# Kernel optimization log

Measured on AMD Instinct MI355X. Metric: run time of the kernel, lower is better.

The kernel has to match this reference:

```python
import jax, jax.numpy as jnp
import numpy as np

SR = 22050
L = 2097153            # output_size = int(SR*95.109); equals NFFT//2+1 so spectral broadcast is well-defined
NFFT = 4194304         # 2**ceil(log2(L))
BANDS = [(1.0, 4.0), (4.0, 8.0), (8.0, 13.0), (13.0, 30.0), (30.0, 100.0), (100.0, 200.0)]
SPEC = [7.83, 528.0, 396.0, 2.5, 14.1, 432.0, 6.0, 30.0]
WIN = 15               # min(15, NFFT//100)
FREQS_NP = np.fft.rfftfreq(NFFT, 1.0 / SR).astype(np.float32)
FREQS = jnp.asarray(FREQS_NP)


def _freq_mod(sig, band_w, freq_w, harm_prog, tm_w1, tm_b1, tm_w2, tm_b2, tm_w3, tm_b3):
    t = jnp.arange(L, dtype=jnp.float32)
    Xf = jnp.fft.rfft(jnp.pad(sig, (0, NFFT - L)))            # [L] complex64
    # sequential band enhancements == product of per-band multipliers
    mult = jnp.ones((L,), jnp.float32)
    for b, (lo, hi) in enumerate(BANDS):
        c = (lo + hi) / 2.0
        w = (hi - lo) / 2.0
        mask = jnp.exp(-0.5 * ((FREQS - c) / (w / 2.0)) ** 2)
        mask = jnp.where((FREQS < lo) | (FREQS > hi), 0.0, mask)
        tmod = jnp.sin(2.0 * np.pi * c * t / SR)
        mult = mult * (1.0 + mask * band_w[b] * (1.0 + 0.2 * tmod))
    # harmonic progression (identical for every specific frequency -> compute once)
    tn = (t / L)[:, None]
    h = jax.nn.relu(tn @ tm_w1 + tm_b1)
    h = jax.nn.relu(h @ tm_w2 + tm_b2)
    mp = h @ tm_w3 + tm_b3                                    # [L, 8]
    chord_idx = jnp.floor(t / L * 8.0).astype(jnp.int32) % 8
    chord = harm_prog[chord_idx] * (1.0 + mp[:, 1] * jnp.sin(2.0 * np.pi * t / L))[:, None]
    prog_mean = chord.mean()
    # specific-frequency harmonic windows (static indices; commutative multiplies)
    smult = jnp.ones((L,), jnp.float32)
    for k, f in enumerate(SPEC):
        for m in (1.0, 2.0, 3.0, 4.0, 5.0):
            hf = f * m
            if hf >= SR / 2:
                continue
            hidx = int(np.argmin(np.abs(FREQS_NP - hf)))
            s = max(0, hidx - WIN)
            e = min(L - 1, hidx + WIN)
            win = jnp.asarray(np.exp(-0.5 * ((np.arange(s, e + 1) - hidx) / (WIN / 3.0)) ** 2).astype(np.float32))
            enh = freq_w[k] * win * (1.0 / m ** 1.2) * (1.0 + prog_mean)
            smult = smult.at[s:e + 1].multiply(1.0 + enh)
    Xf = Xf * mult * smult
    mag = jnp.abs(Xf)
    ph = jnp.angle(Xf)
    mag_s = jnp.concatenate([mag[:1], mag[1:-1] * 0.7 + mag[:-2] * 0.15 + mag[2:] * 0.15, mag[-1:]])
    Xc = mag_s * jnp.exp(1j * ph)
    return jnp.fft.irfft(Xc, n=NFFT)[:L]


def _conv1d(x, w, b, stride):
    y = jax.lax.conv_general_dilated(x, w, (stride,), [(2, 2)], dimension_numbers=("NCH", "OIH", "NCH"))
    return y + b[None, :, None]


def setup_inputs() -> dict:
    key = jax.random.key(0)
    ks = jax.random.split(key, 16)
    n = lambda k, s, sc=1.0: jax.random.normal(k, s, dtype=jnp.float32) * sc
    return {
        "z": n(ks[0], (1, 1, L)),
        "condition": n(ks[1], (1, 8)),
        "band_w": jnp.full((6,), 0.5, jnp.float32),
        "freq_w": jnp.full((8,), 0.3, jnp.float32),
        "harm_prog": n(ks[2], (8, 4)),
        "tm_w1": n(ks[3], (1, 32), 0.5), "tm_b1": jnp.zeros((32,), jnp.float32),
        "tm_w2": n(ks[4], (32, 16), 0.2), "tm_b2": jnp.zeros((16,), jnp.float32),
        "tm_w3": n(ks[5], (16, 8), 0.2), "tm_b3": jnp.zeros((8,), jnp.float32),
        "c1_w": n(ks[6], (32, 1, 5), 0.3), "c1_b": jnp.zeros((32,), jnp.float32),
        "c2_w": n(ks[7], (64, 32, 5), 0.08), "c2_b": jnp.zeros((64,), jnp.float32),
        "c3_w": n(ks[8], (128, 64, 5), 0.05), "c3_b": jnp.zeros((128,), jnp.float32),
        "mx_w1": n(ks[9], (192, 256), 0.07), "mx_b1": jnp.zeros((256,), jnp.float32),
        "mx_w2": n(ks[10], (256, 1), 0.06), "mx_b2": jnp.zeros((1,), jnp.float32),
    }


def reference(z, condition, band_w, freq_w, harm_prog, tm_w1, tm_b1, tm_w2, tm_b2, tm_w3, tm_b3,
              c1_w, c1_b, c2_w, c2_b, c3_w, c3_b, mx_w1, mx_b1, mx_w2, mx_b2):
    base = _freq_mod(z[0, 0], band_w, freq_w, harm_prog, tm_w1, tm_b1, tm_w2, tm_b2, tm_w3, tm_b3)[None, None, :]
    h = jax.nn.leaky_relu(_conv1d(base, c1_w, c1_b, 2), 0.2)
    h = jax.nn.leaky_relu(_conv1d(h, c2_w, c2_b, 2), 0.2)
    h = jax.nn.leaky_relu(_conv1d(h, c3_w, c3_b, 2), 0.2)
    feat = h.mean(axis=2)                                     # [1, 128]
    emb = jnp.zeros((1, 64), jnp.float32)                     # instrument_idx=None path
    mixed = jnp.concatenate([feat, emb], axis=1)              # [1, 192]
    out = jax.nn.leaky_relu(mixed @ mx_w1 + mx_b1, 0.2) @ mx_w2 + mx_b2
    return out
```

## Files before the change

kernel.cpp:

```cpp
#include <hip/hip_runtime.h>
#include <cmath>

#define LSIG  2097153
#define MH    2097152
#define NFFTC 4194304
#define NT128 16384
#define O1C   1048577
#define O2C   524289
#define O3C   262145

#define TO3   62
#define NB3   4229

#define A_OFF    0
#define B_OFF    16777216
#define PM_OFF   58720268
#define FEAT_OFF 58720272
#define W2Q_OFF  50331664
#define W3Q_OFF  50352144
#define W1Q_OFF  50434064

struct SmultTab { int hidx[40]; float inv12[40]; int fk[40]; int maxe; };

typedef short short8 __attribute__((ext_vector_type(8)));
typedef float f32x4v __attribute__((ext_vector_type(4)));

union AFrag { uint4 q; short8 s; };
union BFrag { uint4 q; unsigned int u[4]; short8 s; };

__device__ __forceinline__ float lrelu(float a){ return a > 0.0f ? a : 0.2f*a; }

__device__ __forceinline__ float hsin(float rev){ return __builtin_amdgcn_sinf(rev); }
__device__ __forceinline__ float hcos(float rev){ return __builtin_amdgcn_cosf(rev); }

__device__ __forceinline__ unsigned int rbf(float f) {
  unsigned int u = __float_as_uint(f);
  u += 0x7fffu + ((u >> 16) & 1u);
  return u >> 16;
}
__device__ __forceinline__ unsigned int pack_bf2(float a, float b) {
  unsigned int r;
  asm("v_cvt_pk_bf16_f32 %0, %1, %2" : "=v"(r) : "v"(a), "v"(b));
  return r;
}

__device__ __forceinline__ int swz1(int pos, int dw) {
  return (pos*16 + dw) ^ (((pos >> 1) & 7) << 2);
}
__device__ __forceinline__ int swz2(int pos, int dw) {
  return (pos*32 + dw) ^ (((pos >> 1) & 7) << 2);
}

__device__ __forceinline__ float2 cadd(float2 a, float2 b){ return make_float2(a.x+b.x, a.y+b.y); }
__device__ __forceinline__ float2 csub(float2 a, float2 b){ return make_float2(a.x-b.x, a.y-b.y); }

template<bool FWD> __device__ __forceinline__ float2 jrot(float2 z){
  return FWD ? make_float2(z.y, -z.x) : make_float2(-z.y, z.x);
}

template<bool FWD> __device__ __forceinline__ void dft8(float2 v[8]) {
  const float cq = 0.70710678118654752440f;
  const float S  = FWD ? -1.0f : 1.0f;
  float2 e0 = cadd(v[0], v[4]), e1 = csub(v[0], v[4]);
  float2 e2 = cadd(v[2], v[6]), e3 = csub(v[2], v[6]);
  float2 E0 = cadd(e0, e2), E2 = csub(e0, e2);
  float2 jt = jrot<FWD>(e3);
  float2 E1 = cadd(e1, jt), E3 = csub(e1, jt);
  float2 o0 = cadd(v[1], v[5]), o1 = csub(v[1], v[5]);
  float2 o2 = cadd(v[3], v[7]), o3 = csub(v[3], v[7]);
  float2 O0 = cadd(o0, o2), O2 = csub(o0, o2);
  float2 jo = jrot<FWD>(o3);
  float2 O1 = cadd(o1, jo), O3 = csub(o1, jo);
  float2 w1 = make_float2(cq*O1.x - S*cq*O1.y, cq*O1.y + S*cq*O1.x);
  float2 w2 = jrot<FWD>(O2);
  float2 w3 = make_float2(-cq*O3.x - S*cq*O3.y, -cq*O3.y + S*cq*O3.x);
  v[0] = cadd(E0, O0); v[4] = csub(E0, O0);
  v[1] = cadd(E1, w1); v[5] = csub(E1, w1);
  v[2] = cadd(E2, w2); v[6] = csub(E2, w2);
  v[3] = cadd(E3, w3); v[7] = csub(E3, w3);
}

template<bool FWD>
__device__ __forceinline__ void fft128_body(float2* stage, int t, int jb, int Ns) {
  const float ssg = FWD ? -1.0f : 1.0f;
  const float invden = 1.0f / (float)(128 * Ns);
  {
    const int jj = t >> 4, b = t & 15;
    const int m = (jb + jj) & (Ns - 1);
    float2 v[8];
#pragma unroll
    for (int a = 0; a < 8; ++a) {
      const int r = 16*a + b;
      float2 x = stage[jj*128 + ((r + 9*jj) & 127)];
      if (Ns > 1) {
        float rev = (float)(m * r) * invden;
        float sn = ssg * hsin(rev), cs = hcos(rev);
        x = make_float2(x.x*cs - x.y*sn, x.x*sn + x.y*cs);
      }
      v[a] = x;
    }
    dft8<FWD>(v);
#pragma unroll
    for (int d = 0; d < 8; ++d)
      stage[jj*128 + ((16*d + b + 9*jj) & 127)] = v[d];
  }
  __syncthreads();
  {
    float2 y[16];
    const int jj = (t & 255) >> 3, d = t & 7;
    if (t < 256) {
#pragma unroll
      for (int b = 0; b < 16; ++b) {
        float2 x = stage[jj*128 + ((16*d + b + 9*jj) & 127)];
        float rev = (float)(b*d) * 0.0078125f;
        float sn = ssg * hsin(rev), cs = hcos(rev);
        y[b] = make_float2(x.x*cs - x.y*sn, x.x*sn + x.y*cs);
      }
    }
    __syncthreads();
    if (t < 256) {
      float2 E[8], O[8];
#pragma unroll
      for (int b = 0; b < 8; ++b) { E[b] = y[2*b]; O[b] = y[2*b+1]; }
      dft8<FWD>(E);
      dft8<FWD>(O);
#pragma unroll
      for (int c = 0; c < 8; ++c) {
        float rev = (float)c * 0.0625f;
        float sn = ssg * hsin(rev), cs = hcos(rev);
        float2 To = make_float2(O[c].x*cs - O[c].y*sn, O[c].x*sn + O[c].y*cs);
        stage[jj*128 + ((8*c + d + 9*jj) & 127)]      = cadd(E[c], To);
        stage[jj*128 + ((8*c + 64 + d + 9*jj) & 127)] = csub(E[c], To);
      }
    }
  }
  __syncthreads();
}

template<bool FWD, bool TRUNC>
__global__ __launch_bounds__(512) void kfft128(const float2* __restrict__ src,
                                               float2* __restrict__ dst, int Ns) {
  __shared__ float2 stage[4096];
  const int t = threadIdx.x;
  const int jb = blockIdx.x * 32;
  for (int c = 0; c < 8; ++c) {
    int idx = t + 512*c;
    int jj = idx & 31, rr = idx >> 5;
    stage[jj*128 + ((rr + 9*jj) & 127)] = src[jb + jj + rr*NT128];
  }
  __syncthreads();
  fft128_body<FWD>(stage, t, jb, Ns);
  for (int c = 0; c < 8; ++c) {
    int idx = t + 512*c;
    int jj, k;
    if (Ns == 1) { jj = idx >> 7; k = idx & 127; }
    else         { jj = idx & 31; k = idx >> 5; }
    int j2 = jb + jj, m2 = j2 & (Ns - 1);
    if (TRUNC && !(k < 64 || (k == 64 && j2 == 0))) continue;
    dst[(j2 - m2)*128 + m2 + k*Ns] = stage[jj*128 + ((k + 9*jj) & 127)];
  }
}

__global__ __launch_bounds__(512) void kfirst(
    const float* __restrict__ zin, float2* __restrict__ dst,
    const float* __restrict__ tw1, const float* __restrict__ tb1,
    const float* __restrict__ tw2, const float* __restrict__ tb2,
    const float* __restrict__ tw3, const float* __restrict__ tb3,
    const float* __restrict__ hp, float* __restrict__ pm,
    float* __restrict__ feat) {
  __shared__ float2 stage[4096];
  __shared__ float sw1[32], sb1[32], sw2[512], sb2[16], sw3[16], shp[8], sb31[1];
  __shared__ float red[512];
  const int t = threadIdx.x;
  const int bb = blockIdx.x;
  if (bb < 512) {
    const int jb = bb * 32;
    for (int c = 0; c < 8; ++c) {
      int idx = t + 512*c;
      int jj = idx & 31, rr = idx >> 5;
      int n = jb + jj + rr*NT128;
      float2 a;
      if (n < 1048576)       a = ((const float2*)zin)[n];
      else if (n == 1048576) a = make_float2(zin[2097152], 0.0f);
      else                   a = make_float2(0.0f, 0.0f);
      stage[jj*128 + ((rr + 9*jj) & 127)] = a;
    }
    __syncthreads();
    fft128_body<true>(stage, t, jb, 1);
    for (int c = 0; c < 8; ++c) {
      int idx = t + 512*c;
      int jj = idx >> 7, k = idx & 127;
      dst[(jb + jj)*128 + k] = stage[jj*128 + ((k + 9*jj) & 127)];
    }
    return;
  }
  if (t < 32) { sw1[t] = tw1[t]; sb1[t] = tb1[t]; }
  sw2[t] = tw2[t];
  if (t < 16) { sb2[t] = tb2[t]; sw3[t] = tw3[t*8+1]; }
  if (t < 8) { float s = 0.f; for (int j = 0; j < 4; ++j) s += hp[t*4+j]; shp[t] = s; }
  if (t == 0) sb31[0] = tb3[1];
  __syncthreads();
  const int gid = (bb - 512)*512 + t;
  if (gid < 32768) feat[gid] = 0.0f;
  const float Lf = 2097153.0f;
  float tnv[4], sv[4];
  int ci[4];
  float acc[4][16];
#pragma unroll
  for (int e = 0; e < 4; ++e) {
    float ti = (float)(gid + e*524288);
    float tn = ti / Lf;
    tnv[e] = tn;
    sv[e] = hsin(tn);
    ci[e] = ((int)floorf(tn * 8.0f)) & 7;
#pragma unroll
    for (int kk = 0; kk < 16; ++kk) acc[e][kk] = sb2[kk];
  }
  for (int j = 0; j < 32; ++j) {
    float a = sw1[j], b = sb1[j];
    float hj[4];
#pragma unroll
    for (int e = 0; e < 4; ++e) hj[e] = fmaxf(a*tnv[e] + b, 0.0f);
#pragma unroll
    for (int kk = 0; kk < 16; ++kk) {
      float w = sw2[j*16 + kk];
#pragma unroll
      for (int e = 0; e < 4; ++e) acc[e][kk] += hj[e]*w;
    }
  }
  float lsum = 0.0f;
#pragma unroll
  for (int e = 0; e < 4; ++e) {
    float mp1 = sb31[0];
#pragma unroll
    for (int kk = 0; kk < 16; ++kk) mp1 += fmaxf(acc[e][kk], 0.0f)*sw3[kk];
    lsum += shp[ci[e]] * (1.0f + mp1*sv[e]);
  }
  if (gid == 0) {
    float ti = 2097152.0f;
    float tn = ti / Lf;
    float a1[16];
    for (int kk = 0; kk < 16; ++kk) a1[kk] = sb2[kk];
    for (int j = 0; j < 32; ++j) {
      float h = fmaxf(sw1[j]*tn + sb1[j], 0.0f);
      for (int kk = 0; kk < 16; ++kk) a1[kk] += h*sw2[j*16+kk];
    }
    float mp1 = sb31[0];
    for (int kk = 0; kk < 16; ++kk) mp1 += fmaxf(a1[kk], 0.0f)*sw3[kk];
    float svx = hsin(tn);
    int cix = ((int)floorf(tn * 8.0f)) & 7;
    lsum += shp[cix] * (1.0f + mp1*svx);
  }
  red[t] = lsum;
  __syncthreads();
  for (int off = 256; off > 0; off >>= 1) {
    if (t < off) red[t] += red[t+off];
    __syncthreads();
  }
  if (t == 0) atomicAdd(pm, red[0]);
}

__device__ __forceinline__ float2 xsplit(float2 zk, float2 zm, float rev) {
  float2 s  = make_float2(zk.x + zm.x, zk.y - zm.y);
  float2 dd = make_float2(zk.x - zm.x, zk.y + zm.y);
  float sn = -hsin(rev), cs = hcos(rev);
  float2 t1 = make_float2(cs*dd.x - sn*dd.y, cs*dd.y + sn*dd.x);
  return make_float2(0.5f*(s.x + t1.y), 0.5f*(s.y - t1.x));
}
__device__ __forceinline__ float2 scale_xc(float2 c, float mg, float ms) {
  if (mg > 0.0f) { float sc = ms/mg; return make_float2(c.x*sc, c.y*sc); }
  return make_float2(ms, 0.0f);
}
__device__ __forceinline__ float2 invpack(int n, float2 a, float2 b) {
  float2 s  = make_float2(a.x + b.x, a.y - b.y);
  float2 dd = make_float2(a.x - b.x, a.y + b.y);
  float rev = (float)n * (1.0f / (float)NFFTC);
  float sn = hsin(rev), cs = hcos(rev);
  float2 xo = make_float2(0.5f*(cs*dd.x - sn*dd.y), 0.5f*(cs*dd.y + sn*dd.x));
  const float sc = 1.0f / (float)MH;
  return make_float2((0.5f*s.x - xo.y)*sc, (0.5f*s.y + xo.x)*sc);
}

__global__ __launch_bounds__(256) void kspectral(const float2* __restrict__ Z,
    float2* __restrict__ A, const float* __restrict__ bwp,
    const float* __restrict__ fwp, const float* __restrict__ pm_in, SmultTab tab,
    const float* __restrict__ c1w, const float* __restrict__ c2w,
    const float* __restrict__ c3w, unsigned short* __restrict__ w1q,
    unsigned short* __restrict__ w2q, unsigned short* __restrict__ w3q) {
  const int bb = blockIdx.x;
  const int t = threadIdx.x;
  if (bb >= 4096) {
    int i = (bb - 4096)*256 + t;
    if (i < 1024) {
      int e = i & 7, quad = (i >> 3) & 3, ch = i >> 5;
      float v = (quad == 0 && e < 5) ? c1w[ch*5 + e] : 0.0f;
      w1q[i] = (unsigned short)rbf(v);
    }
    if (i < 10240) {
      int e = i & 7, quad = (i >> 3) & 3, kt = (i >> 5) % 5, ch = i / 160;
      int c1 = quad*8 + e;
      w2q[i] = (unsigned short)rbf(c2w[ch*160 + c1*5 + kt]);
    }
    if (i < 40960) {
      int e = i & 7, quad = (i >> 3) & 3, kt = (i >> 5) % 10, ch = i / 320;
      int c2 = (kt & 1)*32 + quad*8 + e;
      w3q[i] = (unsigned short)rbf(c3w[ch*320 + c2*5 + (kt >> 1)]);
    }
    return;
  }
  __shared__ float2 Xlo[258], Xhi[258];
  __shared__ float  Mlo[258], Mhi[258];
  const int k0 = bb * 256;
  const float pm1 = 1.0f + pm_in[0] * (1.0f/8388612.0f);
  for (int w = t; w < 258; w += 256) {
    int k = k0 - 1 + w;
    float2 zk = Z[k & (MH-1)];
    float2 zm = Z[(MH - k) & (MH-1)];
    {
      float2 X = xsplit(zk, zm, (float)k * (1.0f/(float)NFFTC));
      float mv = 1.0f;
      if (k <= 38050) {
        const float blo[6] = {1.0f,4.0f,8.0f,13.0f,30.0f,100.0f};
        const float bhi[6] = {4.0f,8.0f,13.0f,30.0f,100.0f,200.0f};
        const float bcn[6] = {2.5f,6.0f,10.5f,21.5f,65.0f,150.0f};
        const float bhw[6] = {0.75f,1.0f,1.25f,4.25f,17.5f,25.0f};
        float f = (float)((double)k * (22050.0/4194304.0));
#pragma unroll
        for (int b = 0; b < 6; ++b) {
          if (f >= blo[b] && f <= bhi[b]) {
            float q = (f - bcn[b]) / bhw[b];
            float mask = expf(-0.5f*q*q);
            double frd = (double)k * ((double)bcn[b] / 22050.0);
            frd -= floor(frd);
            float tm = hsin((float)frd);
            mv *= (1.0f + mask * bwp[b] * (1.0f + 0.2f*tm));
          }
        }
      }
      if (k <= tab.maxe) {
        for (int ww = 0; ww < 40; ++ww) {
          int dlt = k - tab.hidx[ww];
          if (dlt >= -15 && dlt <= 15) {
            float x = (float)dlt * 0.2f;
            float win = expf(-0.5f*x*x);
            float enh = fwp[tab.fk[ww]] * win * tab.inv12[ww] * pm1;
            mv *= (1.0f + enh);
          }
        }
      }
      X.x *= mv; X.y *= mv;
      Xlo[w] = X; Mlo[w] = sqrtf(X.x*X.x + X.y*X.y);
    }
    {
      float2 X = xsplit(zm, zk, (float)(MH - k) * (1.0f/(float)NFFTC));
      Xhi[w] = X; Mhi[w] = sqrtf(X.x*X.x + X.y*X.y);
    }
  }
  __syncthreads();
  const int k = k0 + t, w = t + 1;
  float msl = (k == 0) ? Mlo[w] : 0.7f*Mlo[w] + 0.15f*(Mlo[w-1] + Mlo[w+1]);
  float2 xl = scale_xc(Xlo[w], Mlo[w], msl);
  float msh = (k == 0) ? Mhi[w] : 0.7f*Mhi[w] + 0.15f*(Mhi[w+1] + Mhi[w-1]);
  float2 xh = scale_xc(Xhi[w], Mhi[w], msh);
  A[k] = invpack(k, xl, xh);
  if (k >= 1) A[MH - k] = invpack(MH - k, xh, xl);
  if (bb == 4095 && t == 255) {
    float2 Xm = Xlo[257]; float Mm = Mlo[257];
    float ms = 0.7f*Mm + 0.15f*(Mlo[256] + Mhi[256]);
    float2 xm = scale_xc(Xm, Mm, ms);
    A[1048576] = invpack(1048576, xm, xm);
  }
}

__global__ __launch_bounds__(256, 4) void kconv(const float* __restrict__ x,
    const unsigned short* __restrict__ w1q, const unsigned short* __restrict__ w2q,
    const unsigned short* __restrict__ w3q, const float* __restrict__ c1b,
    const float* __restrict__ c2b, const float* __restrict__ c3b,
    float* __restrict__ feat) {
  __shared__ float sb[552];
  __shared__ unsigned int sh1[4352];
  __shared__ unsigned int sh2[4224];
  const int tid  = threadIdx.x;
  const int blk  = blockIdx.x;
  const int s3   = blk * TO3;
  const int lane = tid & 63;
  const int wv   = tid >> 6;
  const int col  = lane & 15;
  const int quad = lane >> 4;

  const uint4* W1 = (const uint4*)w1q;
  AFrag a1w[2];
#pragma unroll
  for (int mi = 0; mi < 2; ++mi)
    a1w[mi].q = W1[(mi*16 + col)*4 + quad];

  const uint4* W2 = (const uint4*)w2q;
  const int mt2 = (wv & 1) * 2;
  const int ntb2 = (wv >> 1) * 4;
  uint4 wk2[2][5];
#pragma unroll
  for (int mi = 0; mi < 2; ++mi)
#pragma unroll
    for (int kt = 0; kt < 5; ++kt)
      wk2[mi][kt] = W2[(((mt2+mi)*16 + col)*5 + kt)*4 + quad];

  float b1r[2][4], b2r[2][4];
#pragma unroll
  for (int mi = 0; mi < 2; ++mi)
#pragma unroll
    for (int r = 0; r < 4; ++r) {
      b1r[mi][r] = c1b[mi*16 + quad*4 + r];
      b2r[mi][r] = c2b[(mt2+mi)*16 + quad*4 + r];
    }

  {
    const int pb = 8*s3 - 14;
    for (int idx = tid; idx < 552; idx += 256) {
      int p = pb + idx;
      sb[idx] = (idx < 517 && p >= 0 && p < LSIG) ? x[p] : 0.0f;
    }
    if (tid < 128) sh2[4096 + tid] = 0u;
  }
  __syncthreads();

  {
    const int a1 = 4*s3 - 6;
    for (int nt = wv; nt < 17; nt += 4) {
      const int n = nt*16 + col;
      BFrag bf;
      if (quad == 0) {
        const float* ps = &sb[2*n];
        bf.u[0] = pack_bf2(ps[0], ps[1]);
        bf.u[1] = pack_bf2(ps[2], ps[3]);
        bf.u[2] = pack_bf2(ps[4], ps[5]);
        bf.u[3] = pack_bf2(ps[6], ps[7]);
      } else {
        bf.u[0] = 0u; bf.u[1] = 0u; bf.u[2] = 0u; bf.u[3] = 0u;
      }
      f32x4v acc[2];
      acc[0] = (f32x4v){b1r[0][0], b1r[0][1], b1r[0][2], b1r[0][3]};
      acc[1] = (f32x4v){b1r[1][0], b1r[1][1], b1r[1][2], b1r[1][3]};
      acc[0] = __builtin_amdgcn_mfma_f32_16x16x32_bf16(a1w[0].s, bf.s, acc[0], 0, 0, 0);
      acc[1] = __builtin_amdgcn_mfma_f32_16x16x32_bf16(a1w[1].s, bf.s, acc[1], 0, 0, 0);
      const int o1 = a1 + n;
      const bool ok = (n <= 257) && (o1 >= 0) && (o1 < O1C);
#pragma unroll
      for (int mi = 0; mi < 2; ++mi) {
        float v0 = ok ? lrelu(acc[mi][0]) : 0.0f;
        float v1 = ok ? lrelu(acc[mi][1]) : 0.0f;
        float v2 = ok ? lrelu(acc[mi][2]) : 0.0f;
        float v3 = ok ? lrelu(acc[mi][3]) : 0.0f;
        uint2 pk; pk.x = pack_bf2(v0, v1); pk.y = pack_bf2(v2, v3);
        *(uint2*)&sh1[swz1(n, mi*8 + quad*2)] = pk;
      }
    }
  }
  __syncthreads();

  f32x4v acc2[2][4];
#pragma unroll
  for (int mi = 0; mi < 2; ++mi)
#pragma unroll
    for (int nt = 0; nt < 4; ++nt)
      acc2[mi][nt] = (f32x4v){b2r[mi][0], b2r[mi][1], b2r[mi][2], b2r[mi][3]};
#pragma unroll
  for (int kt = 0; kt < 5; ++kt) {
#pragma unroll
    for (int nt = 0; nt < 4; ++nt) {
      const int n = (ntb2 + nt)*16 + col;
      const int row = 2*n + kt;
      BFrag bf;
      bf.q = *(const uint4*)&sh1[swz1(row, quad*4)];
      AFrag a0, a1; a0.q = wk2[0][kt]; a1.q = wk2[1][kt];
      acc2[0][nt] = __builtin_amdgcn_mfma_f32_16x16x32_bf16(a0.s, bf.s, acc2[0][nt], 0, 0, 0);
      acc2[1][nt] = __builtin_amdgcn_mfma_f32_16x16x32_bf16(a1.s, bf.s, acc2[1][nt], 0, 0, 0);
    }
  }

  {
    const int a2 = 2*s3 - 2;
#pragma unroll
    for (int nt = 0; nt < 4; ++nt) {
      const int p = (ntb2 + nt)*16 + col;
      const int o2 = a2 + p;
      const bool ok = (o2 >= 0) && (o2 < O2C);
#pragma unroll
      for (int mi = 0; mi < 2; ++mi) {
        float v0 = ok ? lrelu(acc2[mi][nt][0]) : 0.0f;
        float v1 = ok ? lrelu(acc2[mi][nt][1]) : 0.0f;
        float v2 = ok ? lrelu(acc2[mi][nt][2]) : 0.0f;
        float v3 = ok ? lrelu(acc2[mi][nt][3]) : 0.0f;
        const int dwb = (mt2+mi)*8 + quad*2;
        uint2 pk; pk.x = pack_bf2(v0, v1); pk.y = pack_bf2(v2, v3);
        *(uint2*)&sh2[swz2(p, dwb)] = pk;
      }
    }
  }
  __syncthreads();

  {
    const uint4* W3 = (const uint4*)w3q;
    const int slot = (blk & 255) * 128;
#pragma unroll
    for (int pass = 0; pass < 2; ++pass) {
      const int mt = wv + 4*pass;
      uint4 wk3[10];
#pragma unroll
      for (int kt = 0; kt < 10; ++kt)
        wk3[kt] = W3[((mt*16 + col)*10 + kt)*4 + quad];
      float b3r[4];
#pragma unroll
      for (int r = 0; r < 4; ++r) b3r[r] = c3b[mt*16 + quad*4 + r];
      f32x4v acc3[4];
#pragma unroll
      for (int nt = 0; nt < 4; ++nt)
        acc3[nt] = (f32x4v){b3r[0], b3r[1], b3r[2], b3r[3]};
#pragma unroll
      for (int kt = 0; kt < 10; ++kt) {
        const int tap = kt >> 1;
        const int hh  = (kt & 1) * 16;
#pragma unroll
        for (int nt = 0; nt < 4; ++nt) {
          const int n = nt*16 + col;
          const int row = 2*n + tap;
          BFrag bf;
          bf.q = *(const uint4*)&sh2[swz2(row, hh + quad*4)];
          AFrag a; a.q = wk3[kt];
          acc3[nt] = __builtin_amdgcn_mfma_f32_16x16x32_bf16(a.s, bf.s, acc3[nt], 0, 0, 0);
        }
      }
#pragma unroll
      for (int r = 0; r < 4; ++r) {
        const int ch = mt*16 + quad*4 + r;
        float v = 0.0f;
#pragma unroll
        for (int nt = 0; nt < 4; ++nt) {
          const int n = nt*16 + col;
          const bool ok = (n < TO3) && (s3 + n < O3C);
          if (ok) v += lrelu(acc3[nt][r]);
        }
        v += __shfl_xor(v, 1);
        v += __shfl_xor(v, 2);
        v += __shfl_xor(v, 4);
        v += __shfl_xor(v, 8);
        if (col == 0) atomicAdd(&feat[slot + ch], v);
      }
    }
  }
}

__global__ __launch_bounds__(256) void kfinal(const float* __restrict__ feat,
    const float* __restrict__ mw1, const float* __restrict__ mb1,
    const float* __restrict__ mw2, const float* __restrict__ mb2,
    float* __restrict__ out) {
  __shared__ float sfeat[128];
  __shared__ float red[256];
  const int tid = threadIdx.x;
  if (tid < 128) {
    float s = 0.0f;
    for (int sl = 0; sl < 256; ++sl) s += feat[sl*128 + tid];
    sfeat[tid] = s / 262145.0f;
  }
  __syncthreads();
  float y = mb1[tid];
  for (int i = 0; i < 128; ++i) y += sfeat[i] * mw1[i*256 + tid];
  y = y > 0.0f ? y : 0.2f*y;
  red[tid] = y * mw2[tid];
  __syncthreads();
  for (int off = 128; off > 0; off >>= 1) {
    if (tid < off) red[tid] += red[tid+off];
    __syncthreads();
  }
  if (tid == 0) out[0] = red[0] + mb2[0];
}

extern "C" void kernel_launch(void* const* d_in, const int* in_sizes, int n_in,
                              void* d_out, int out_size, void* d_ws, size_t ws_size,
                              hipStream_t stream) {
  (void)in_sizes; (void)n_in; (void)out_size; (void)ws_size;
  const float* z   = (const float*)d_in[0];
  const float* bw  = (const float*)d_in[2];
  const float* fw  = (const float*)d_in[3];
  const float* hp  = (const float*)d_in[4];
  const float* tw1 = (const float*)d_in[5];
  const float* tb1 = (const float*)d_in[6];
  const float* tw2 = (const float*)d_in[7];
  const float* tb2 = (const float*)d_in[8];
  const float* tw3 = (const float*)d_in[9];
  const float* tb3 = (const float*)d_in[10];
  const float* c1w = (const float*)d_in[11];
  const float* c1b = (const float*)d_in[12];
  const float* c2w = (const float*)d_in[13];
  const float* c2b = (const float*)d_in[14];
  const float* c3w = (const float*)d_in[15];
  const float* c3b = (const float*)d_in[16];
  const float* mw1 = (const float*)d_in[17];
  const float* mb1 = (const float*)d_in[18];
  const float* mw2 = (const float*)d_in[19];
  const float* mb2 = (const float*)d_in[20];

  char* wsb = (char*)d_ws;
  float2* A    = (float2*)(wsb + A_OFF);
  float2* B    = (float2*)(wsb + B_OFF);
  float*  PM   = (float*)(wsb + PM_OFF);
  float*  FEAT = (float*)(wsb + FEAT_OFF);
  unsigned short* W1Q = (unsigned short*)(wsb + W1Q_OFF);
  unsigned short* W2Q = (unsigned short*)(wsb + W2Q_OFF);
  unsigned short* W3Q = (unsigned short*)(wsb + W3Q_OFF);

  SmultTab tab;
  {
    const double spec[8] = {7.83, 528.0, 396.0, 2.5, 14.1, 432.0, 6.0, 30.0};
    int n = 0, maxe = 0;
    for (int kk = 0; kk < 8; ++kk)
      for (int m = 1; m <= 5; ++m) {
        double hf = spec[kk] * (double)m;
        if (hf >= 11025.0) continue;
        int hidx = (int)std::floor(hf * (4194304.0/22050.0) + 0.5);
        tab.hidx[n]  = hidx;
        tab.inv12[n] = (float)(1.0/std::pow((double)m, 1.2));
        tab.fk[n]    = kk;
        if (hidx + 15 > maxe) maxe = hidx + 15;
        ++n;
      }
    tab.maxe = maxe;
  }

  (void)hipMemsetAsync(wsb + PM_OFF, 0, 4, stream);

  kfirst<<<1536,512,0,stream>>>(z, A, tw1,tb1,tw2,tb2,tw3,tb3,hp, PM, FEAT);

  kfft128<true,false><<<512,512,0,stream>>>(A, B, 128);
  kfft128<true,false><<<512,512,0,stream>>>(B, A, 16384);

  kspectral<<<4256,256,0,stream>>>(A, B, bw, fw, PM, tab, c1w, c2w, c3w, W1Q, W2Q, W3Q);

  kfft128<false,false><<<512,512,0,stream>>>(B, A, 1);
  kfft128<false,false><<<512,512,0,stream>>>(A, B, 128);
  kfft128<false,true ><<<512,512,0,stream>>>(B, A, 16384);

  kconv<<<NB3,256,0,stream>>>((const float*)A, W1Q, W2Q, W3Q, c1b, c2b, c3b, FEAT);
  kfinal<<<1,256,0,stream>>>(FEAT, mw1, mb1, mw2, mb2, (float*)d_out);
}
```

Baseline: 278.8 us.

## Fuse two inverse FFT passes into one 16K-point shared-memory kernel with transposed spectral output

The spectral kernel now handles 2048 bins per block and writes its inverse-packed output in transposed column order. A new 1024-thread kernel can then run a full 16384-point inverse FFT per column entirely in a 128 KB shared-memory tile, replacing two separate global-memory passes. Shared-memory slot indexing in the existing FFT kernels also gains an XOR swizzle to reduce bank conflicts. This removes one full read and write of the 4M-point complex array. In exchange, only 128 blocks run with one block per CU, which can leave the GPU underoccupied, and the transposed scattered writes may coalesce poorly.

```diff
diff --git a/kernel.cpp b/kernel.cpp
--- a/kernel.cpp
+++ b/kernel.cpp
@@ -49,6 +49,15 @@
 }
 __device__ __forceinline__ int swz2(int pos, int dw) {
   return (pos*32 + dw) ^ (((pos >> 1) & 7) << 2);
+}
+
+__device__ __forceinline__ int slot128(int jj, int q) {
+  int s = q ^ ((q >> 4) & 7);
+  return jj*128 + ((s + 9*jj) & 127);
+}
+__device__ __forceinline__ int phys16k(int x) {
+  int hi = x >> 7, lo = x & 127;
+  return hi*128 + (((lo + 9*hi) & 127) ^ ((hi >> 4) & 7));
 }
 
 __device__ __forceinline__ float2 cadd(float2 a, float2 b){ return make_float2(a.x+b.x, a.y+b.y); }
@@ -91,7 +100,7 @@
 #pragma unroll
     for (int a = 0; a < 8; ++a) {
       const int r = 16*a + b;
-      float2 x = stage[jj*128 + ((r + 9*jj) & 127)];
+      float2 x = stage[slot128(jj, r)];
       if (Ns > 1) {
         float rev = (float)(m * r) * invden;
         float sn = ssg * hsin(rev), cs = hcos(rev);
@@ -102,7 +111,7 @@
     dft8<FWD>(v);
 #pragma unroll
     for (int d = 0; d < 8; ++d)
-      stage[jj*128 + ((16*d + b + 9*jj) & 127)] = v[d];
+      stage[slot128(jj, 16*d + b)] = v[d];
   }
   __syncthreads();
   {
@@ -111,7 +120,7 @@
     if (t < 256) {
 #pragma unroll
       for (int b = 0; b < 16; ++b) {
-        float2 x = stage[jj*128 + ((16*d + b + 9*jj) & 127)];
+        float2 x = stage[slot128(jj, 16*d + b)];
         float rev = (float)(b*d) * 0.0078125f;
         float sn = ssg * hsin(rev), cs = hcos(rev);
         y[b] = make_float2(x.x*cs - x.y*sn, x.x*sn + x.y*cs);
@@ -129,8 +138,8 @@
         float rev = (float)c * 0.0625f;
         float sn = ssg * hsin(rev), cs = hcos(rev);
         float2 To = make_float2(O[c].x*cs - O[c].y*sn, O[c].x*sn + O[c].y*cs);
-        stage[jj*128 + ((8*c + d + 9*jj) & 127)]      = cadd(E[c], To);
-        stage[jj*128 + ((8*c + 64 + d + 9*jj) & 127)] = csub(E[c], To);
+        stage[slot128(jj, 8*c + d)]      = cadd(E[c], To);
+        stage[slot128(jj, 8*c + 64 + d)] = csub(E[c], To);
       }
     }
   }
@@ -146,7 +155,7 @@
   for (int c = 0; c < 8; ++c) {
     int idx = t + 512*c;
     int jj = idx & 31, rr = idx >> 5;
-    stage[jj*128 + ((rr + 9*jj) & 127)] = src[jb + jj + rr*NT128];
+    stage[slot128(jj, rr)] = src[jb + jj + rr*NT128];
   }
   __syncthreads();
   fft128_body<FWD>(stage, t, jb, Ns);
@@ -157,7 +166,105 @@
     else         { jj = idx & 31; k = idx >> 5; }
     int j2 = jb + jj, m2 = j2 & (Ns - 1);
     if (TRUNC && !(k < 64 || (k == 64 && j2 == 0))) continue;
-    dst[(j2 - m2)*128 + m2 + k*Ns] = stage[jj*128 + ((k + 9*jj) & 127)];
+    dst[(j2 - m2)*128 + m2 + k*Ns] = stage[slot128(jj, k)];
+  }
+}
+
+__global__ __launch_bounds__(1024, 1) void kmegai(const float2* __restrict__ src,
+                                                  float2* __restrict__ dst) {
+  __shared__ float2 L[16384];
+  const int t = threadIdx.x;
+  const int c = blockIdx.x;
+  const float2* col = src + c*16384;
+  for (int i = 0; i < 16; ++i) {
+    int x = t + 1024*i;
+    L[phys16k(x)] = col[x];
+  }
+  __syncthreads();
+#pragma unroll
+  for (int u0 = 0; u0 < 2; ++u0) {
+    int u = t + 1024*u0;
+    int p = u >> 4, b = u & 15;
+    float2 v[8];
+#pragma unroll
+    for (int a = 0; a < 8; ++a) v[a] = L[phys16k(p + 128*(16*a + b))];
+    dft8<false>(v);
+#pragma unroll
+    for (int d = 0; d < 8; ++d) L[phys16k(p + 128*(16*d + b))] = v[d];
+  }
+  __syncthreads();
+  {
+    int p = t >> 3, d = t & 7;
+    float2 y[16];
+#pragma unroll
+    for (int b = 0; b < 16; ++b) {
+      float2 x = L[phys16k(p + 128*(16*d + b))];
+      float rev = (float)(b*d) * 0.0078125f;
+      float sn = hsin(rev), cs = hcos(rev);
+      y[b] = make_float2(x.x*cs - x.y*sn, x.x*sn + x.y*cs);
+    }
+    __syncthreads();
+    float2 E[8], O[8];
+#pragma unroll
+    for (int b = 0; b < 8; ++b) { E[b] = y[2*b]; O[b] = y[2*b+1]; }
+    dft8<false>(E); dft8<false>(O);
+#pragma unroll
+    for (int cc = 0; cc < 8; ++cc) {
+      float rev = (float)cc * 0.0625f;
+      float sn = hsin(rev), cs = hcos(rev);
+      float2 To = make_float2(O[cc].x*cs - O[cc].y*sn, O[cc].x*sn + O[cc].y*cs);
+      L[phys16k(p + 128*(8*cc + d))]      = cadd(E[cc], To);
+      L[phys16k(p + 128*(8*cc + 64 + d))] = csub(E[cc], To);
+    }
+  }
+  __syncthreads();
+#pragma unroll
+  for (int u0 = 0; u0 < 2; ++u0) {
+    int u = t + 1024*u0;
+    int k2 = u >> 4, b = u & 15;
+    float2 v[8];
+#pragma unroll
+    for (int a = 0; a < 8; ++a) {
+      int r = 16*a + b;
+      float2 x = L[phys16k(r + 128*k2)];
+      float rev = (float)(k2*r) * (1.0f/16384.0f);
+      float sn = hsin(rev), cs = hcos(rev);
+      v[a] = make_float2(x.x*cs - x.y*sn, x.x*sn + x.y*cs);
+    }
+    dft8<false>(v);
+#pragma unroll
+    for (int d = 0; d < 8; ++d) L[phys16k((16*d + b) + 128*k2)] = v[d];
+  }
+  __syncthreads();
+  {
+    int k2 = t >> 3, d = t & 7;
+    float2 y[16];
+#pragma unroll
+    for (int b = 0; b < 16; ++b) {
+      float2 x = L[phys16k((16*d + b) + 128*k2)];
+      float rev = (float)(b*d) * 0.0078125f;
+      float sn = hsin(rev), cs = hcos(rev);
+      y[b] = make_float2(x.x*cs - x.y*sn, x.x*sn + x.y*cs);
+    }
+    __syncthreads();
+    float2 E[8], O[8];
+#pragma unroll
+    for (int b = 0; b < 8; ++b) { E[b] = y[2*b]; O[b] = y[2*b+1]; }
+    dft8<false>(E); dft8<false>(O);
+#pragma unroll
+    for (int cc = 0; cc < 8; ++cc) {
+      float rev = (float)cc * 0.0625f;
+      float sn = hsin(rev), cs = hcos(rev);
+      float2 To = make_float2(O[cc].x*cs - O[cc].y*sn, O[cc].x*sn + O[cc].y*cs);
+      L[phys16k(k2 + 128*(8*cc + d))]      = cadd(E[cc], To);
+      L[phys16k(k2 + 128*(8*cc + 64 + d))] = csub(E[cc], To);
+    }
+  }
+  __syncthreads();
+  float2* out = dst + c*16384;
+  for (int i = 0; i < 16; ++i) {
+    int g = t + 1024*i;
+    out[g] = L[phys16k(g)];
   }
 }
 
@@ -183,14 +290,14 @@
       if (n < 1048576)       a = ((const float2*)zin)[n];
       else if (n == 1048576) a = make_float2(zin[2097152], 0.0f);
       else                   a = make_float2(0.0f, 0.0f);
-      stage[jj*128 + ((rr + 9*jj) & 127)] = a;
+      stage[slot128(jj, rr)] = a;
     }
     __syncthreads();
     fft128_body<true>(stage, t, jb, 1);
     for (int c = 0; c < 8; ++c) {
       int idx = t + 512*c;
       int jj = idx >> 7, k = idx & 127;
-      dst[(jb + jj)*128 + k] = stage[jj*128 + ((k + 9*jj) & 127)];
+      dst[(jb + jj)*128 + k] = stage[slot128(jj, k)];
     }
     return;
   }
@@ -281,16 +388,18 @@
   return make_float2((0.5f*s.x - xo.y)*sc, (0.5f*s.y + xo.x)*sc);
 }
 
+__device__ __forceinline__ int xw(int w){ return w + (w >> 7); }
+
 __global__ __launch_bounds__(256) void kspectral(const float2* __restrict__ Z,
-    float2* __restrict__ A, const float* __restrict__ bwp,
+    float2* __restrict__ YT, const float* __restrict__ bwp,
     const float* __restrict__ fwp, const float* __restrict__ pm_in, SmultTab tab,
     const float* __restrict__ c1w, const float* __restrict__ c2w,
     const float* __restrict__ c3w, unsigned short* __restrict__ w1q,
     unsigned short* __restrict__ w2q, unsigned short* __restrict__ w3q) {
   const int bb = blockIdx.x;
   const int t = threadIdx.x;
-  if (bb >= 4096) {
-    int i = (bb - 4096)*256 + t;
+  if (bb >= 512) {
+    int i = (bb - 512)*256 + t;
     if (i < 1024) {
       int e = i & 7, quad = (i >> 3) & 3, ch = i >> 5;
       float v = (quad == 0 && e < 5) ? c1w[ch*5 + e] : 0.0f;
@@ -308,11 +417,11 @@
     }
     return;
   }
-  __shared__ float2 Xlo[258], Xhi[258];
-  __shared__ float  Mlo[258], Mhi[258];
-  const int k0 = bb * 256;
+  __shared__ float2 Xlo[2067], Xhi[2067];
+  __shared__ float  Mlo[2050], Mhi[2050];
+  const int k0 = bb * 2048;
   const float pm1 = 1.0f + pm_in[0] * (1.0f/8388612.0f);
-  for (int w = t; w < 258; w += 256) {
+  for (int w = t; w < 2050; w += 256) {
     int k = k0 - 1 + w;
     float2 zk = Z[k & (MH-1)];
     float2 zm = Z[(MH - k) & (MH-1)];
@@ -349,26 +458,44 @@
         }
       }
       X.x *= mv; X.y *= mv;
-      Xlo[w] = X; Mlo[w] = sqrtf(X.x*X.x + X.y*X.y);
+      Xlo[xw(w)] = X; Mlo[w] = sqrtf(X.x*X.x + X.y*X.y);
     }
     {
       float2 X = xsplit(zm, zk, (float)(MH - k) * (1.0f/(float)NFFTC));
-      Xhi[w] = X; Mhi[w] = sqrtf(X.x*X.x + X.y*X.y);
-    }
-  }
-  __syncthreads();
-  const int k = k0 + t, w = t + 1;
-  float msl = (k == 0) ? Mlo[w] : 0.7f*Mlo[w] + 0.15f*(Mlo[w-1] + Mlo[w+1]);
-  float2 xl = scale_xc(Xlo[w], Mlo[w], msl);
-  float msh = (k == 0) ? Mhi[w] : 0.7f*Mhi[w] + 0.15f*(Mhi[w+1] + Mhi[w-1]);
-  float2 xh = scale_xc(Xhi[w], Mhi[w], msh);
-  A[k] = invpack(k, xl, xh);
-  if (k >= 1) A[MH - k] = invpack(MH - k, xh, xl);
-  if (bb == 4095 && t == 255) {
-    float2 Xm = Xlo[257]; float Mm = Mlo[257];
-    float ms = 0.7f*Mm + 0.15f*(Mlo[256] + Mhi[256]);
-    float2 xm = scale_xc(Xm, Mm, ms);
-    A[1048576] = invpack(1048576, xm, xm);
+      Xhi[xw(w)] = X; Mhi[w] = sqrtf(X.x*X.x + X.y*X.y);
+    }
+  }
+  __syncthreads();
+  for (int rr = 0; rr < 8; ++rr) {
+    const int w = 1 + t + 256*rr;
+    const int k = k0 + w - 1;
+    float msl = (k == 0) ? Mlo[w] : 0.7f*Mlo[w] + 0.15f*(Mlo[w-1] + Mlo[w+1]);
+    float2 xl = scale_xc(Xlo[xw(w)], Mlo[w], msl);
+    float msh = (k == 0) ? Mhi[w] : 0.7f*Mhi[w] + 0.15f*(Mhi[w+1] + Mhi[w-1]);
+    float2 xh = scale_xc(Xhi[xw(w)], Mhi[w], msh);
+    Xlo[xw(w)] = invpack(k, xl, xh);
+    Xhi[xw(w)] = invpack(MH - k, xh, xl);
+  }
+  if (bb == 511 && t == 255) {
+    float Mm = Mlo[2049];
+    float ms = 0.7f*Mm + 0.15f*(Mlo[2048] + Mhi[2048]);
+    float2 xm = scale_xc(Xlo[xw(2049)], Mm, ms);
+    YT[8192] = invpack(1048576, xm, xm);
+  }
+  __syncthreads();
+  const int q0 = k0 >> 7;
+  for (int ii = t; ii < 2048; ii += 256) {
+    int cc = ii >> 4, qq = ii & 15;
+    YT[cc*16384 + q0 + qq] = Xlo[xw(1 + cc + 128*qq)];
+  }
+  const int qh0 = (MH - k0 - 2048) >> 7;
+  for (int ii = t; ii < 2048; ii += 256) {
+    int cc = ii >> 4, qq = ii & 15;
+    int jdx = 128*qq + ((cc + 127) & 127);
+    if (bb == 0 && jdx == 2047) continue;
+    int w = 2048 - jdx;
+    int qh = qh0 + qq + (cc == 0 ? 1 : 0);
+    YT[cc*16384 + qh] = Xhi[xw(w)];
   }
 }
 
@@ -633,12 +760,11 @@
   kfft128<true,false><<<512,512,0,stream>>>(A, B, 128);
   kfft128<true,false><<<512,512,0,stream>>>(B, A, 16384);
 
-  kspectral<<<4256,256,0,stream>>>(A, B, bw, fw, PM, tab, c1w, c2w, c3w, W1Q, W2Q, W3Q);
-
-  kfft128<false,false><<<512,512,0,stream>>>(B, A, 1);
-  kfft128<false,false><<<512,512,0,stream>>>(A, B, 128);
-  kfft128<false,true ><<<512,512,0,stream>>>(B, A, 16384);
-
-  kconv<<<NB3,256,0,stream>>>((const float*)A, W1Q, W2Q, W3Q, c1b, c2b, c3b, FEAT);
+  kspectral<<<672,256,0,stream>>>(A, B, bw, fw, PM, tab, c1w, c2w, c3w, W1Q, W2Q, W3Q);
+
+  kmegai<<<128,1024,0,stream>>>(B, A);
+  kfft128<false,true><<<512,512,0,stream>>>(A, B, 16384);
+
+  kconv<<<NB3,256,0,stream>>>((const float*)B, W1Q, W2Q, W3Q, c1b, c2b, c3b, FEAT);
   kfinal<<<1,256,0,stream>>>(FEAT, mw1, mb1, mw2, mb2, (float*)d_out);
 }
```

After: 301.1 us. +8.0%, slower.
